# Kernel optimization log

Measured on AMD Instinct MI355X. Metric: run time of the kernel, lower is better.

## Reference

```python
import jax, jax.numpy as jnp
import numpy as np

OBS_DIM, ACT_DIM = 512, 32
H1, H2 = 1024, 1024
BATCH = 4096
LOG2PI = float(np.log(2.0 * np.pi))


def setup_inputs() -> dict:
    key = jax.random.key(0)
    ks = jax.random.split(key, 9)
    def uinit(k, shape, fan_in):
        b = 1.0 / np.sqrt(fan_in)
        return jax.random.uniform(k, shape, jnp.float32, -b, b)
    return {
        "obs": jax.random.normal(ks[0], (BATCH, OBS_DIM), jnp.float32),
        "act": jax.random.normal(ks[1], (BATCH, ACT_DIM), jnp.float32),
        # stacked per-head weights: [act_dim, in, out]
        "W1": uinit(ks[2], (ACT_DIM, OBS_DIM, H1), OBS_DIM),
        "b1": uinit(ks[3], (ACT_DIM, H1), OBS_DIM),
        "W2": uinit(ks[4], (ACT_DIM, H1, H2), H1),
        "b2": uinit(ks[5], (ACT_DIM, H2), H1),
        "W3": uinit(ks[6], (ACT_DIM, H2), H2),   # out dim 1, squeezed
        "b3": uinit(ks[7], (ACT_DIM,), H2),
        "log_std": jnp.full((ACT_DIM,), -0.5, jnp.float32),
    }


def reference(obs, act, W1, b1, W2, b2, W3, b3, log_std):
    # act_dim decoupled 3-layer MLPs as batched GEMMs over the head axis 'a'
    x = jnp.tanh(jnp.einsum('bo,aoh->bah', obs, W1) + b1)          # [B, A, H1]
    x = jnp.tanh(jnp.einsum('bah,ahk->bak', x, W2) + b2)           # [B, A, H2]
    mu = jnp.einsum('bak,ak->ba', x, W3) + b3                      # [B, A]
    # diagonal Normal log_prob(act).sum(-1)
    z = (act - mu) * jnp.exp(-log_std)
    logp = jnp.sum(-0.5 * (z * z + LOG2PI) - log_std, axis=-1)     # [B]
    return (mu, logp)
```

## Files before the change

### kernel.cpp

```cpp
#include <hip/hip_runtime.h>
#include <hip/hip_bf16.h>

typedef unsigned short u16;
typedef __bf16 bf16x8 __attribute__((ext_vector_type(8)));
typedef float f32x4 __attribute__((ext_vector_type(4)));

#define LOG2PI_F 1.8378770664093453f

__device__ __forceinline__ u16 f2bf(float f) {
  union { __hip_bfloat16 h; u16 u; } cvt;
  cvt.h = __float2bfloat16(f);
  return cvt.u;
}

__device__ __forceinline__ float fast_tanh(float x) {
  float e = __expf(2.0f * x);
  return 1.0f - 2.0f * __builtin_amdgcn_rcpf(e + 1.0f);
}

__device__ __forceinline__ void load_lds16(const void* g, void* l) {
  __builtin_amdgcn_global_load_lds(
      (const __attribute__((address_space(1))) void*)g,
      (__attribute__((address_space(3))) void*)l,
      16, 0, 0);
}

__global__ void cvt_f32_bf16(const float* __restrict__ in, u16* __restrict__ out, int n4) {
  int i = blockIdx.x * blockDim.x + threadIdx.x;
  int stride = gridDim.x * blockDim.x;
  for (int j = i; j < n4; j += stride) {
    float4 v = reinterpret_cast<const float4*>(in)[j];
    ushort4 o;
    o.x = f2bf(v.x); o.y = f2bf(v.y); o.z = f2bf(v.z); o.w = f2bf(v.w);
    reinterpret_cast<ushort4*>(out)[j] = o;
  }
}

__global__ void transpose_cvt(const float* __restrict__ W, u16* __restrict__ Wt,
                              int K, int N) {
  __shared__ u16 t[64][66];
  const int a = blockIdx.z;
  const int n0 = blockIdx.x * 64, k0 = blockIdx.y * 64;
  const float* Wh = W + (size_t)a * K * N;
  u16* Wth = Wt + (size_t)a * N * K;
  const int tid = threadIdx.x;
#pragma unroll
  for (int j = 0; j < 16; ++j) {
    int idx = j * 256 + tid;
    int r = idx >> 6, c = idx & 63;
    t[r][c] = f2bf(Wh[(size_t)(k0 + r) * N + n0 + c]);
  }
  __syncthreads();
#pragma unroll
  for (int j = 0; j < 16; ++j) {
    int idx = j * 256 + tid;
    int r = idx >> 6, c = idx & 63;
    Wth[(size_t)(n0 + r) * K + k0 + c] = t[c][r];
  }
}

template <int MODE>
__global__ __launch_bounds__(256, 2) void gemm_heads(
    const u16* __restrict__ A, long aHeadStride,
    const u16* __restrict__ Bt,
    const float* __restrict__ bias,
    int M, int N, int K,
    u16* __restrict__ outBf,
    const float* __restrict__ W3,
    float* __restrict__ muAcc) {
  __shared__ __align__(16) u16 As[128 * 64];
  __shared__ __align__(16) u16 Bs[128 * 64];

  const int tid = threadIdx.x;
  const int l = tid & 63;
  const int w = tid >> 6;
  const int wm = w >> 1, wn = w & 1;
  const int lh = l & 15, lg = l >> 4;

  const int a = blockIdx.z;
  const int m0 = blockIdx.y * 128;
  const int n0 = blockIdx.x * 128;

  const u16* Ah = A + (size_t)a * (size_t)aHeadStride;
  const u16* Bh = Bt + (size_t)a * (size_t)N * (size_t)K;

  f32x4 acc[4][4] = {};

  for (int kt = 0; kt < K; kt += 64) {
#pragma unroll
    for (int i = 0; i < 4; ++i) {
      const int c = i * 256 + tid;
      const int row = c >> 3;
      const int k8 = (c & 7) * 8;
      load_lds16(Ah + (size_t)(m0 + row) * K + kt + k8, &As[c * 8]);
    }
#pragma unroll
    for (int i = 0; i < 4; ++i) {
      const int c = i * 256 + tid;
      const int row = c >> 3;
      const int k8 = (c & 7) * 8;
      load_lds16(Bh + (size_t)(n0 + row) * K + kt + k8, &Bs[c * 8]);
    }
    __syncthreads();

#pragma unroll
    for (int ks = 0; ks < 2; ++ks) {
      bf16x8 af[4], bfr[4];
#pragma unroll
      for (int mf = 0; mf < 4; ++mf)
        af[mf] = *reinterpret_cast<const bf16x8*>(
            &As[(wm * 64 + mf * 16 + lh) * 64 + ks * 32 + lg * 8]);
#pragma unroll
      for (int nf = 0; nf < 4; ++nf)
        bfr[nf] = *reinterpret_cast<const bf16x8*>(
            &Bs[(wn * 64 + nf * 16 + lh) * 64 + ks * 32 + lg * 8]);
#pragma unroll
      for (int mf = 0; mf < 4; ++mf)
#pragma unroll
        for (int nf = 0; nf < 4; ++nf)
          acc[mf][nf] = __builtin_amdgcn_mfma_f32_16x16x32_bf16(
              af[mf], bfr[nf], acc[mf][nf], 0, 0, 0);
    }
    __syncthreads();
  }

  if (MODE == 1) {
    u16* Oh = outBf + (size_t)a * (size_t)M * (size_t)N;
#pragma unroll
    for (int mf = 0; mf < 4; ++mf) {
#pragma unroll
      for (int r = 0; r < 4; ++r) {
        const int row = m0 + wm * 64 + mf * 16 + lg * 4 + r;
#pragma unroll
        for (int nf = 0; nf < 4; ++nf) {
          const int col = n0 + wn * 64 + nf * 16 + lh;
          float v = acc[mf][nf][r] + bias[a * N + col];
          Oh[(size_t)row * N + col] = f2bf(fast_tanh(v));
        }
      }
    }
  } else {
#pragma unroll
    for (int mf = 0; mf < 4; ++mf) {
#pragma unroll
      for (int r = 0; r < 4; ++r) {
        const int row = m0 + wm * 64 + mf * 16 + lg * 4 + r;
        float p = 0.f;
#pragma unroll
        for (int nf = 0; nf < 4; ++nf) {
          const int col = n0 + wn * 64 + nf * 16 + lh;
          float v = acc[mf][nf][r] + bias[a * N + col];
          p += fast_tanh(v) * W3[a * N + col];
        }
        p += __shfl_xor(p, 1);
        p += __shfl_xor(p, 2);
        p += __shfl_xor(p, 4);
        p += __shfl_xor(p, 8);
        if (lh == 0) atomicAdd(&muAcc[(size_t)row * 32 + a], p);
      }
    }
  }
}

__global__ void finalize_kernel(const float* __restrict__ muAcc,
                                const float* __restrict__ b3,
                                const float* __restrict__ lstd,
                                const float* __restrict__ act,
                                float* __restrict__ out, int M) {
  int b = blockIdx.x * 256 + threadIdx.x;
  if (b >= M) return;
  float lp = 0.f;
#pragma unroll
  for (int a = 0; a < 32; ++a) {
    float mu = muAcc[(size_t)b * 32 + a] + b3[a];
    out[(size_t)b * 32 + a] = mu;
    float ls = lstd[a];
    float z = (act[(size_t)b * 32 + a] - mu) * __expf(-ls);
    lp += -0.5f * (z * z + LOG2PI_F) - ls;
  }
  out[(size_t)M * 32 + b] = lp;
}

extern "C" void kernel_launch(void* const* d_in, const int* in_sizes, int n_in,
                              void* d_out, int out_size, void* d_ws, size_t ws_size,
                              hipStream_t stream) {
  const float* obs = (const float*)d_in[0];
  const float* act = (const float*)d_in[1];
  const float* W1 = (const float*)d_in[2];
  const float* b1 = (const float*)d_in[3];
  const float* W2 = (const float*)d_in[4];
  const float* b2 = (const float*)d_in[5];
  const float* W3 = (const float*)d_in[6];
  const float* b3 = (const float*)d_in[7];
  const float* lstd = (const float*)d_in[8];

  constexpr int B = 4096, OBS = 512, A = 32, H1 = 1024, H2 = 1024;

  u16* obs_bf = (u16*)d_ws;
  u16* W1t = obs_bf + (size_t)B * OBS;
  u16* W2t = W1t + (size_t)A * H1 * OBS;
  u16* x1 = W2t + (size_t)A * H2 * H1;
  float* muAcc = (float*)(x1 + (size_t)A * B * H1);
  float* out = (float*)d_out;

  hipMemsetAsync(muAcc, 0, (size_t)B * A * sizeof(float), stream);

  cvt_f32_bf16<<<1024, 256, 0, stream>>>(obs, obs_bf, B * OBS / 4);
  transpose_cvt<<<dim3(H1 / 64, OBS / 64, A), 256, 0, stream>>>(W1, W1t, OBS, H1);
  transpose_cvt<<<dim3(H2 / 64, H1 / 64, A), 256, 0, stream>>>(W2, W2t, H1, H2);

  gemm_heads<1><<<dim3(H1 / 128, B / 128, A), 256, 0, stream>>>(
      obs_bf, 0L, W1t, b1, B, H1, OBS, x1, nullptr, nullptr);

  gemm_heads<2><<<dim3(H2 / 128, B / 128, A), 256, 0, stream>>>(
      x1, (long)B * H1, W2t, b2, B, H2, H1, nullptr, W3, muAcc);

  finalize_kernel<<<B / 256, 256, 0, stream>>>(muAcc, b3, lstd, act, out, B);
}
```

Before: 897.1 us.

## Use 256x256 tiles with double-buffered LDS, XOR swizzle, and XCD-aware block mapping

Replaces the 128x128 per-head GEMM with a 256x256-tile, 512-thread kernel. The new kernel double-buffers LDS loads so the next K-tile arrives while the current one computes, and XOR-swizzles LDS columns to avoid bank conflicts. It remaps the flat block id across the 8 XCDs so blocks sharing a head are grouped on the same die, and raises MFMA priority with s_setprio. This targets global-to-LDS latency and LDS bandwidth stalls, at the cost of larger register/LDS footprint (128KB LDS per block) that may limit occupancy.

```diff
diff --git a/kernel.cpp b/kernel.cpp
--- a/kernel.cpp
+++ b/kernel.cpp
@@ -60,103 +60,137 @@
 }
 
 template <int MODE>
-__global__ __launch_bounds__(256, 2) void gemm_heads(
+__global__ __launch_bounds__(512, 2) void gemm256(
     const u16* __restrict__ A, long aHeadStride,
     const u16* __restrict__ Bt,
     const float* __restrict__ bias,
-    int M, int N, int K,
+    int M, int N, int K, int gridN,
     u16* __restrict__ outBf,
     const float* __restrict__ W3,
     float* __restrict__ muAcc) {
-  __shared__ __align__(16) u16 As[128 * 64];
-  __shared__ __align__(16) u16 Bs[128 * 64];
+  __shared__ __align__(16) u16 lds[2][2][256 * 64];
 
   const int tid = threadIdx.x;
-  const int l = tid & 63;
-  const int w = tid >> 6;
-  const int wm = w >> 1, wn = w & 1;
+  const int w = tid >> 6, l = tid & 63;
+  const int wm = w >> 2, wn = w & 3;
   const int lh = l & 15, lg = l >> 4;
 
-  const int a = blockIdx.z;
-  const int m0 = blockIdx.y * 128;
-  const int n0 = blockIdx.x * 128;
-
-  const u16* Ah = A + (size_t)a * (size_t)aHeadStride;
-  const u16* Bh = Bt + (size_t)a * (size_t)N * (size_t)K;
-
-  f32x4 acc[4][4] = {};
-
-  for (int kt = 0; kt < K; kt += 64) {
+  const int nwg = gridDim.x;
+  const int cpx = nwg >> 3;
+  int bid = (blockIdx.x & 7) * cpx + (blockIdx.x >> 3);
+  const int bph = (M >> 8) * gridN;
+  const int head = bid / bph;
+  const int rem = bid % bph;
+  const int m0 = (rem / gridN) << 8;
+  const int n0 = (rem % gridN) << 8;
+
+  const u16* Ah = A + (size_t)head * (size_t)aHeadStride;
+  const u16* Bh = Bt + (size_t)head * (size_t)N * (size_t)K;
+
+  auto stage = [&](int buf, int kt) {
 #pragma unroll
     for (int i = 0; i < 4; ++i) {
-      const int c = i * 256 + tid;
-      const int row = c >> 3;
-      const int k8 = (c & 7) * 8;
-      load_lds16(Ah + (size_t)(m0 + row) * K + kt + k8, &As[c * 8]);
+      int c = i * 512 + tid;
+      int row = c >> 3, j = c & 7;
+      int js = j ^ (row & 7);
+      load_lds16(Ah + (size_t)(m0 + row) * K + kt + js * 8, &lds[buf][0][c * 8]);
     }
 #pragma unroll
     for (int i = 0; i < 4; ++i) {
-      const int c = i * 256 + tid;
-      const int row = c >> 3;
-      const int k8 = (c & 7) * 8;
-      load_lds16(Bh + (size_t)(n0 + row) * K + kt + k8, &Bs[c * 8]);
-    }
-    __syncthreads();
+      int c = i * 512 + tid;
+      int row = c >> 3, j = c & 7;
+      int js = j ^ (row & 7);
+      load_lds16(Bh + (size_t)(n0 + row) * K + kt + js * 8, &lds[buf][1][c * 8]);
+    }
+  };
+
+  f32x4 acc[8][4] = {};
+  const int NT = K >> 6;
+
+  stage(0, 0);
+  stage(1, 64);
+  asm volatile("s_waitcnt vmcnt(8)" ::: "memory");
+  __builtin_amdgcn_sched_barrier(0);
+  __builtin_amdgcn_s_barrier();
+
+  for (int t = 0; t < NT; ++t) {
+    const u16* As = lds[t & 1][0];
+    const u16* Bs = lds[t & 1][1];
 
 #pragma unroll
     for (int ks = 0; ks < 2; ++ks) {
-      bf16x8 af[4], bfr[4];
-#pragma unroll
-      for (int mf = 0; mf < 4; ++mf)
-        af[mf] = *reinterpret_cast<const bf16x8*>(
-            &As[(wm * 64 + mf * 16 + lh) * 64 + ks * 32 + lg * 8]);
-#pragma unroll
-      for (int nf = 0; nf < 4; ++nf)
-        bfr[nf] = *reinterpret_cast<const bf16x8*>(
-            &Bs[(wn * 64 + nf * 16 + lh) * 64 + ks * 32 + lg * 8]);
-#pragma unroll
-      for (int mf = 0; mf < 4; ++mf)
-#pragma unroll
-        for (int nf = 0; nf < 4; ++nf)
-          acc[mf][nf] = __builtin_amdgcn_mfma_f32_16x16x32_bf16(
-              af[mf], bfr[nf], acc[mf][nf], 0, 0, 0);
-    }
-    __syncthreads();
+      bf16x8 bfr[4];
+#pragma unroll
+      for (int nf = 0; nf < 4; ++nf) {
+        int row = wn * 64 + nf * 16 + lh;
+        int j = (ks * 4 + lg) ^ (lh & 7);
+        bfr[nf] = *reinterpret_cast<const bf16x8*>(&Bs[row * 64 + j * 8]);
+      }
+#pragma unroll
+      for (int mfh = 0; mfh < 2; ++mfh) {
+        bf16x8 af[4];
+#pragma unroll
+        for (int mi = 0; mi < 4; ++mi) {
+          int row = wm * 128 + (mfh * 4 + mi) * 16 + lh;
+          int j = (ks * 4 + lg) ^ (lh & 7);
+          af[mi] = *reinterpret_cast<const bf16x8*>(&As[row * 64 + j * 8]);
+        }
+        __builtin_amdgcn_s_setprio(1);
+#pragma unroll
+        for (int mi = 0; mi < 4; ++mi)
+#pragma unroll
+          for (int nf = 0; nf < 4; ++nf)
+            acc[mfh * 4 + mi][nf] = __builtin_amdgcn_mfma_f32_16x16x32_bf16(
+                af[mi], bfr[nf], acc[mfh * 4 + mi][nf], 0, 0, 0);
+        __builtin_amdgcn_s_setprio(0);
+        __builtin_amdgcn_s_barrier();
+      }
+    }
+
+    __builtin_amdgcn_sched_barrier(0);
+    if (t + 2 < NT) {
+      stage(t & 1, (t + 2) << 6);
+      asm volatile("s_waitcnt vmcnt(8)" ::: "memory");
+    } else {
+      asm volatile("s_waitcnt vmcnt(0)" ::: "memory");
+    }
+    __builtin_amdgcn_sched_barrier(0);
+    __builtin_amdgcn_s_barrier();
   }
 
   if (MODE == 1) {
-    u16* Oh = outBf + (size_t)a * (size_t)M * (size_t)N;
-#pragma unroll
-    for (int mf = 0; mf < 4; ++mf) {
-#pragma unroll
-      for (int r = 0; r < 4; ++r) {
-        const int row = m0 + wm * 64 + mf * 16 + lg * 4 + r;
+    u16* Oh = outBf + (size_t)head * (size_t)M * (size_t)N;
+#pragma unroll
+    for (int mf = 0; mf < 8; ++mf) {
+#pragma unroll
+      for (int ri = 0; ri < 4; ++ri) {
+        const int rowg = m0 + wm * 128 + mf * 16 + lg * 4 + ri;
 #pragma unroll
         for (int nf = 0; nf < 4; ++nf) {
           const int col = n0 + wn * 64 + nf * 16 + lh;
-          float v = acc[mf][nf][r] + bias[a * N + col];
-          Oh[(size_t)row * N + col] = f2bf(fast_tanh(v));
+          float v = acc[mf][nf][ri] + bias[head * N + col];
+          Oh[(size_t)rowg * N + col] = f2bf(fast_tanh(v));
         }
       }
     }
   } else {
 #pragma unroll
-    for (int mf = 0; mf < 4; ++mf) {
-#pragma unroll
-      for (int r = 0; r < 4; ++r) {
-        const int row = m0 + wm * 64 + mf * 16 + lg * 4 + r;
+    for (int mf = 0; mf < 8; ++mf) {
+#pragma unroll
+      for (int ri = 0; ri < 4; ++ri) {
+        const int rowg = m0 + wm * 128 + mf * 16 + lg * 4 + ri;
         float p = 0.f;
 #pragma unroll
         for (int nf = 0; nf < 4; ++nf) {
           const int col = n0 + wn * 64 + nf * 16 + lh;
-          float v = acc[mf][nf][r] + bias[a * N + col];
-          p += fast_tanh(v) * W3[a * N + col];
+          float v = acc[mf][nf][ri] + bias[head * N + col];
+          p += fast_tanh(v) * W3[head * N + col];
         }
         p += __shfl_xor(p, 1);
         p += __shfl_xor(p, 2);
         p += __shfl_xor(p, 4);
         p += __shfl_xor(p, 8);
-        if (lh == 0) atomicAdd(&muAcc[(size_t)row * 32 + a], p);
+        if (lh == 0) atomicAdd(&muAcc[(size_t)rowg * 32 + head], p);
       }
     }
   }
@@ -209,11 +243,11 @@
   transpose_cvt<<<dim3(H1 / 64, OBS / 64, A), 256, 0, stream>>>(W1, W1t, OBS, H1);
   transpose_cvt<<<dim3(H2 / 64, H1 / 64, A), 256, 0, stream>>>(W2, W2t, H1, H2);
 
-  gemm_heads<1><<<dim3(H1 / 128, B / 128, A), 256, 0, stream>>>(
-      obs_bf, 0L, W1t, b1, B, H1, OBS, x1, nullptr, nullptr);
-
-  gemm_heads<2><<<dim3(H2 / 128, B / 128, A), 256, 0, stream>>>(
-      x1, (long)B * H1, W2t, b2, B, H2, H1, nullptr, W3, muAcc);
+  gemm256<1><<<(B / 256) * (H1 / 256) * A, 512, 0, stream>>>(
+      obs_bf, 0L, W1t, b1, B, H1, OBS, H1 / 256, x1, nullptr, nullptr);
+
+  gemm256<2><<<(B / 256) * (H2 / 256) * A, 512, 0, stream>>>(
+      x1, (long)B * H1, W2t, b2, B, H2, H1, H2 / 256, nullptr, W3, muAcc);
 
   finalize_kernel<<<B / 256, 256, 0, stream>>>(muAcc, b3, lstd, act, out, B);
 }
```

Measured after the change: 813.1 us. 9.4% less time.

## Swizzle LDS tiles with XOR and remap blocks to XCDs per head

Applied to the files above, without the earlier changes.

Applies an XOR swizzle to the 16-byte chunk index in the LDS A/B tiles so the MFMA fragment reads stop hitting the same banks. It also flattens the grid to 1D and remaps block IDs so consecutive logical tiles land on the same XCD (blockIdx & 7 chiplet interleave). This keeps a head's weight tiles and activation rows within one XCD's L2. The change adds integer index math per block and relies on the grid size being divisible by 8.

```diff
diff --git a/kernel.cpp b/kernel.cpp
--- a/kernel.cpp
+++ b/kernel.cpp
@@ -64,7 +64,7 @@
     const u16* __restrict__ A, long aHeadStride,
     const u16* __restrict__ Bt,
     const float* __restrict__ bias,
-    int M, int N, int K,
+    int M, int N, int K, int gridN,
     u16* __restrict__ outBf,
     const float* __restrict__ W3,
     float* __restrict__ muAcc) {
@@ -77,12 +77,16 @@
   const int wm = w >> 1, wn = w & 1;
   const int lh = l & 15, lg = l >> 4;
 
-  const int a = blockIdx.z;
-  const int m0 = blockIdx.y * 128;
-  const int n0 = blockIdx.x * 128;
-
-  const u16* Ah = A + (size_t)a * (size_t)aHeadStride;
-  const u16* Bh = Bt + (size_t)a * (size_t)N * (size_t)K;
+  const int cpx = gridDim.x >> 3;
+  const int bid = (blockIdx.x & 7) * cpx + (blockIdx.x >> 3);
+  const int bph = (M >> 7) * gridN;
+  const int head = bid / bph;
+  const int rem = bid % bph;
+  const int m0 = (rem / gridN) << 7;
+  const int n0 = (rem % gridN) << 7;
+
+  const u16* Ah = A + (size_t)head * (size_t)aHeadStride;
+  const u16* Bh = Bt + (size_t)head * (size_t)N * (size_t)K;
 
   f32x4 acc[4][4] = {};
 
@@ -90,16 +94,16 @@
 #pragma unroll
     for (int i = 0; i < 4; ++i) {
       const int c = i * 256 + tid;
-      const int row = c >> 3;
-      const int k8 = (c & 7) * 8;
-      load_lds16(Ah + (size_t)(m0 + row) * K + kt + k8, &As[c * 8]);
+      const int row = c >> 3, j = c & 7;
+      const int js = j ^ (row & 7);
+      load_lds16(Ah + (size_t)(m0 + row) * K + kt + js * 8, &As[c * 8]);
     }
 #pragma unroll
     for (int i = 0; i < 4; ++i) {
       const int c = i * 256 + tid;
-      const int row = c >> 3;
-      const int k8 = (c & 7) * 8;
-      load_lds16(Bh + (size_t)(n0 + row) * K + kt + k8, &Bs[c * 8]);
+      const int row = c >> 3, j = c & 7;
+      const int js = j ^ (row & 7);
+      load_lds16(Bh + (size_t)(n0 + row) * K + kt + js * 8, &Bs[c * 8]);
     }
     __syncthreads();
 
@@ -107,13 +111,17 @@
     for (int ks = 0; ks < 2; ++ks) {
       bf16x8 af[4], bfr[4];
 #pragma unroll
-      for (int mf = 0; mf < 4; ++mf)
-        af[mf] = *reinterpret_cast<const bf16x8*>(
-            &As[(wm * 64 + mf * 16 + lh) * 64 + ks * 32 + lg * 8]);
-#pragma unroll
-      for (int nf = 0; nf < 4; ++nf)
-        bfr[nf] = *reinterpret_cast<const bf16x8*>(
-            &Bs[(wn * 64 + nf * 16 + lh) * 64 + ks * 32 + lg * 8]);
+      for (int mf = 0; mf < 4; ++mf) {
+        const int row = wm * 64 + mf * 16 + lh;
+        const int j = (ks * 4 + lg) ^ (lh & 7);
+        af[mf] = *reinterpret_cast<const bf16x8*>(&As[row * 64 + j * 8]);
+      }
+#pragma unroll
+      for (int nf = 0; nf < 4; ++nf) {
+        const int row = wn * 64 + nf * 16 + lh;
+        const int j = (ks * 4 + lg) ^ (lh & 7);
+        bfr[nf] = *reinterpret_cast<const bf16x8*>(&Bs[row * 64 + j * 8]);
+      }
 #pragma unroll
       for (int mf = 0; mf < 4; ++mf)
 #pragma unroll
@@ -125,7 +133,7 @@
   }
 
   if (MODE == 1) {
-    u16* Oh = outBf + (size_t)a * (size_t)M * (size_t)N;
+    u16* Oh = outBf + (size_t)head * (size_t)M * (size_t)N;
 #pragma unroll
     for (int mf = 0; mf < 4; ++mf) {
 #pragma unroll
@@ -134,7 +142,7 @@
 #pragma unroll
         for (int nf = 0; nf < 4; ++nf) {
           const int col = n0 + wn * 64 + nf * 16 + lh;
-          float v = acc[mf][nf][r] + bias[a * N + col];
+          float v = acc[mf][nf][r] + bias[head * N + col];
           Oh[(size_t)row * N + col] = f2bf(fast_tanh(v));
         }
       }
@@ -149,14 +157,14 @@
 #pragma unroll
         for (int nf = 0; nf < 4; ++nf) {
           const int col = n0 + wn * 64 + nf * 16 + lh;
-          float v = acc[mf][nf][r] + bias[a * N + col];
-          p += fast_tanh(v) * W3[a * N + col];
+          float v = acc[mf][nf][r] + bias[head * N + col];
+          p += fast_tanh(v) * W3[head * N + col];
         }
         p += __shfl_xor(p, 1);
         p += __shfl_xor(p, 2);
         p += __shfl_xor(p, 4);
         p += __shfl_xor(p, 8);
-        if (lh == 0) atomicAdd(&muAcc[(size_t)row * 32 + a], p);
+        if (lh == 0) atomicAdd(&muAcc[(size_t)row * 32 + head], p);
       }
     }
   }
@@ -209,11 +217,11 @@
   transpose_cvt<<<dim3(H1 / 64, OBS / 64, A), 256, 0, stream>>>(W1, W1t, OBS, H1);
   transpose_cvt<<<dim3(H2 / 64, H1 / 64, A), 256, 0, stream>>>(W2, W2t, H1, H2);
 
-  gemm_heads<1><<<dim3(H1 / 128, B / 128, A), 256, 0, stream>>>(
-      obs_bf, 0L, W1t, b1, B, H1, OBS, x1, nullptr, nullptr);
-
-  gemm_heads<2><<<dim3(H2 / 128, B / 128, A), 256, 0, stream>>>(
-      x1, (long)B * H1, W2t, b2, B, H2, H1, nullptr, W3, muAcc);
+  gemm_heads<1><<<(B / 128) * (H1 / 128) * A, 256, 0, stream>>>(
+      obs_bf, 0L, W1t, b1, B, H1, OBS, H1 / 128, x1, nullptr, nullptr);
+
+  gemm_heads<2><<<(B / 128) * (H2 / 128) * A, 256, 0, stream>>>(
+      x1, (long)B * H1, W2t, b2, B, H2, H1, H2 / 128, nullptr, W3, muAcc);
 
   finalize_kernel<<<B / 256, 256, 0, stream>>>(muAcc, b3, lstd, act, out, B);
 }
```

Result: faster. 723.6 us (-19.3%).
